# Kernel tuning notes

Measured on AMD Instinct MI355X. Metric: run time of the kernel, lower is better.

Reference implementation:

```python
import itertools
import jax, jax.numpy as jnp
import numpy as np

# static block configuration
B, C, H, W, DIM, HEADS = 2, 4, 60, 120, 512, 8
WS = (2, 6, 12)          # window size (Wc, Wh, Ww)
SS = (1, 3, 6)           # shift size
N = WS[0] * WS[1] * WS[2]            # 144 tokens per window
C1, H1, W1 = C // WS[0], H // WS[1], W // WS[2]
NW = C1 * H1 * W1                    # windows per sample
DH = DIM // HEADS
EPS = 1e-6


def _attn_bias():
    """Static shifted-window attention bias (nW, N, N): 0 within group, -inf across.
    Mirrors compute_3d_shifted_window_mask (warped=True, longitude wrap merge)."""
    img = np.zeros((C, H, W), np.int32)
    c_sl = ((0, C - WS[0]), (C - WS[0], C - SS[0]), (C - SS[0], C))
    h_sl = ((0, H - WS[1]), (H - WS[1], H - SS[1]), (H - SS[1], H))
    w_sl = ((0, W - WS[2]), (W - WS[2], W - SS[2]), (W - SS[2], W))
    cnt = 0
    for (cs, ce), (hs, he), (ws_, we) in itertools.product(c_sl, h_sl, w_sl):
        img[cs:ce, hs:he, ws_:we] = cnt
        cnt += 1
    # warped (periodic longitude) group merges
    for i in range(3):
        for a, b in ((1, 2), (4, 5), (7, 8)):
            img[img == a + 9 * i] = b + 9 * i
    m = img.reshape(C1, WS[0], H1, WS[1], W1, WS[2])
    m = m.transpose(0, 2, 4, 1, 3, 5).reshape(NW, N)
    diff = m[:, None, :] - m[:, :, None]
    return jnp.asarray(np.where(diff != 0, -np.inf, 0.0).astype(np.float32))


_BIAS = _attn_bias()[None, :, None, :, :]  # (1, nW, 1, N, N)


def _ln(x, s, b):
    mu = x.mean(-1, keepdims=True)
    var = x.var(-1, keepdims=True)
    return (x - mu) / jnp.sqrt(var + EPS) * s + b


def setup_inputs() -> dict:
    key = jax.random.key(0)
    ks = jax.random.split(key, 6)
    s = 0.02
    return {
        "x": jax.random.normal(ks[0], (B, C * H * W, DIM), jnp.float32),
        "qkv_w": jax.random.normal(ks[1], (DIM, 3 * DIM), jnp.float32) * s,
        "qkv_b": jnp.zeros((3 * DIM,), jnp.float32),
        "proj_w": jax.random.normal(ks[2], (DIM, DIM), jnp.float32) * s,
        "proj_b": jnp.zeros((DIM,), jnp.float32),
        "norm1_scale": jnp.ones((DIM,), jnp.float32),
        "norm1_bias": jnp.zeros((DIM,), jnp.float32),
        "norm2_scale": jnp.ones((DIM,), jnp.float32),
        "norm2_bias": jnp.zeros((DIM,), jnp.float32),
        "mlp_w1": jax.random.normal(ks[3], (DIM, 4 * DIM), jnp.float32) * s,
        "mlp_b1": jnp.zeros((4 * DIM,), jnp.float32),
        "mlp_w2": jax.random.normal(ks[4], (4 * DIM, DIM), jnp.float32) * s,
        "mlp_b2": jnp.zeros((DIM,), jnp.float32),
    }


def reference(x, qkv_w, qkv_b, proj_w, proj_b, norm1_scale, norm1_bias,
              norm2_scale, norm2_bias, mlp_w1, mlp_b1, mlp_w2, mlp_b2):
    shortcut = x                                   # (B, L, D)
    h = _ln(x, norm1_scale, norm1_bias).reshape(B, C, H, W, DIM)
    # cyclic shift
    h = jnp.roll(h, (-SS[0], -SS[1], -SS[2]), axis=(1, 2, 3))
    # window partition: (B,C,H,W,D) -> (B*nW, N, D)
    h = h.reshape(B, C1, WS[0], H1, WS[1], W1, WS[2], DIM)
    h = h.transpose(0, 1, 3, 5, 2, 4, 6, 7).reshape(B * NW, N, DIM)
    # windowed multi-head self-attention
    qkv = h @ qkv_w + qkv_b                        # (B*nW, N, 3*D)
    qkv = qkv.reshape(B, NW, N, 3, HEADS, DH)
    q = qkv[..., 0, :, :].transpose(0, 1, 3, 2, 4)  # (B, nW, H, N, Dh)
    k = qkv[..., 1, :, :].transpose(0, 1, 3, 2, 4)
    v = qkv[..., 2, :, :].transpose(0, 1, 3, 2, 4)
    scale = 1.0 / float(np.sqrt(DH))
    attn = jnp.einsum("bwhnd,bwhmd->bwhnm", q, k) * scale + _BIAS
    attn = jax.nn.softmax(attn, axis=-1)
    o = jnp.einsum("bwhnm,bwhmd->bwhnd", attn, v)
    o = o.transpose(0, 1, 3, 2, 4).reshape(B * NW, N, DIM)
    o = o @ proj_w + proj_b
    # window reverse: (B*nW, N, D) -> (B,C,H,W,D)
    o = o.reshape(B, C1, H1, W1, WS[0], WS[1], WS[2], DIM)
    o = o.transpose(0, 1, 4, 2, 5, 3, 6, 7).reshape(B, C, H, W, DIM)
    # reverse cyclic shift
    o = jnp.roll(o, SS, axis=(1, 2, 3))
    x = shortcut + o.reshape(B, C * H * W, DIM)    # drop_path is identity
    # MLP block
    h2 = _ln(x, norm2_scale, norm2_bias)
    h2 = jax.nn.gelu(h2 @ mlp_w1 + mlp_b1) @ mlp_w2 + mlp_b2
    return x + h2
```

## Files before the change

### kernel.cpp

```cpp
#include <hip/hip_runtime.h>

typedef __attribute__((ext_vector_type(8))) short bf16x8;
typedef __attribute__((ext_vector_type(4))) float f32x4;
typedef __attribute__((ext_vector_type(8))) unsigned short u16x8;

__device__ inline unsigned short f2bf(float f) {
  unsigned int u = __float_as_uint(f);
  u += 0x7fffu + ((u >> 16) & 1u);
  return (unsigned short)(u >> 16);
}

__device__ inline void gload_lds16(const void* g, void* l) {
  __builtin_amdgcn_global_load_lds(
      (const __attribute__((address_space(1))) void*)g,
      (__attribute__((address_space(3))) void*)l, 16, 0, 0);
}

__global__ void wtrans(const float* __restrict__ W, unsigned short* __restrict__ Wt,
                       int K, int N) {
  int idx = blockIdx.x * 256 + threadIdx.x;
  if (idx >= K * N) return;
  int k = idx / N, n = idx - k * N;
  Wt[(size_t)n * K + k] = f2bf(W[idx]);
}

template <int MODE>
__global__ void ln_k(const float* __restrict__ x, const float* __restrict__ sc,
                     const float* __restrict__ bi, unsigned short* __restrict__ o) {
  int t = blockIdx.x * 4 + (threadIdx.x >> 6);
  int l = threadIdx.x & 63;
  size_t src;
  if (MODE == 0) {
    int b = t / 28800, r = t - b * 28800;
    int win = r / 144, tok = r - win * 144;
    int c1 = win / 100, rem = win - c1 * 100;
    int h1 = rem / 10, w1 = rem - h1 * 10;
    int tc = tok / 72, tr = tok - tc * 72;
    int th = tr / 12, tw = tr - th * 12;
    int cs = c1 * 2 + tc, hs = h1 * 6 + th, wsp = w1 * 12 + tw;
    int co = (cs + 1) & 3;
    int ho = hs + 3; if (ho >= 60) ho -= 60;
    int wo = wsp + 6; if (wo >= 120) wo -= 120;
    src = ((size_t)b * 28800 + (co * 60 + ho) * 120 + wo) * 512;
  } else {
    src = (size_t)t * 512;
  }
  const float4* xr = (const float4*)(x + src);
  float4 v0 = xr[l * 2], v1 = xr[l * 2 + 1];
  float s = v0.x + v0.y + v0.z + v0.w + v1.x + v1.y + v1.z + v1.w;
  float s2 = v0.x * v0.x + v0.y * v0.y + v0.z * v0.z + v0.w * v0.w +
             v1.x * v1.x + v1.y * v1.y + v1.z * v1.z + v1.w * v1.w;
  #pragma unroll
  for (int o2 = 32; o2; o2 >>= 1) {
    s += __shfl_xor(s, o2);
    s2 += __shfl_xor(s2, o2);
  }
  float mean = s * (1.0f / 512.0f);
  float var = s2 * (1.0f / 512.0f) - mean * mean;
  float inv = rsqrtf(var + 1e-6f);
  const float4* scp = (const float4*)sc;
  const float4* bip = (const float4*)bi;
  float4 sa = scp[l * 2], sb = scp[l * 2 + 1];
  float4 ba = bip[l * 2], bb = bip[l * 2 + 1];
  u16x8 ov;
  ov[0] = f2bf((v0.x - mean) * inv * sa.x + ba.x);
  ov[1] = f2bf((v0.y - mean) * inv * sa.y + ba.y);
  ov[2] = f2bf((v0.z - mean) * inv * sa.z + ba.z);
  ov[3] = f2bf((v0.w - mean) * inv * sa.w + ba.w);
  ov[4] = f2bf((v1.x - mean) * inv * sb.x + bb.x);
  ov[5] = f2bf((v1.y - mean) * inv * sb.y + bb.y);
  ov[6] = f2bf((v1.z - mean) * inv * sb.z + bb.z);
  ov[7] = f2bf((v1.w - mean) * inv * sb.w + bb.w);
  *(u16x8*)&o[(size_t)t * 512 + l * 8] = ov;
}

template <int EPI>
__launch_bounds__(256)
__global__ void gemm128(const unsigned short* __restrict__ A,
                        const unsigned short* __restrict__ Bt,
                        const float* __restrict__ bias, void* __restrict__ outp,
                        const float* __restrict__ res, int M, int N, int K) {
  __shared__ __attribute__((aligned(16))) unsigned short As[128 * 32];
  __shared__ __attribute__((aligned(16))) unsigned short Bs[128 * 32];
  int tid = threadIdx.x;
  int w = tid >> 6, l = tid & 63;
  int ntile = N >> 7;
  int bm = blockIdx.x / ntile, bn = blockIdx.x - bm * ntile;
  const unsigned short* Ab = A + (size_t)bm * 128 * K;
  const unsigned short* Bb = Bt + (size_t)bn * 128 * K;
  int lr = l >> 2, lc = (l & 3) << 3;
  int lane15 = l & 15, lk = (l >> 4) << 3;
  int wr = (w >> 1) << 6, wc = (w & 1) << 6;
  f32x4 acc[4][4] = {};
  for (int k0 = 0; k0 < K; k0 += 32) {
    #pragma unroll
    for (int i = 0; i < 2; ++i) {
      int row = i * 64 + w * 16 + lr;
      gload_lds16(Ab + (size_t)row * K + k0 + lc, &As[(i * 64 + w * 16) * 32]);
      gload_lds16(Bb + (size_t)row * K + k0 + lc, &Bs[(i * 64 + w * 16) * 32]);
    }
    __syncthreads();
    bf16x8 af[4], bf[4];
    #pragma unroll
    for (int mt = 0; mt < 4; ++mt)
      af[mt] = *(const bf16x8*)&As[(wr + mt * 16 + lane15) * 32 + lk];
    #pragma unroll
    for (int nt = 0; nt < 4; ++nt)
      bf[nt] = *(const bf16x8*)&Bs[(wc + nt * 16 + lane15) * 32 + lk];
    #pragma unroll
    for (int mt = 0; mt < 4; ++mt)
      #pragma unroll
      for (int nt = 0; nt < 4; ++nt)
        acc[mt][nt] =
            __builtin_amdgcn_mfma_f32_16x16x32_bf16(af[mt], bf[nt], acc[mt][nt], 0, 0, 0);
    __syncthreads();
  }
  float* outf = (float*)outp;
  unsigned short* outh = (unsigned short*)outp;
  #pragma unroll
  for (int mt = 0; mt < 4; ++mt) {
    #pragma unroll
    for (int j = 0; j < 4; ++j) {
      int grow = bm * 128 + wr + mt * 16 + ((l >> 4) << 2) + j;
      int win = 0, tok = 0;
      size_t rowbase = 0;
      if constexpr (EPI == 0) {
        win = grow / 144;
        tok = grow - win * 144;
      } else if constexpr (EPI == 1) {
        win = grow / 144;
        tok = grow - win * 144;
        int b = win / 200, wl = win - b * 200;
        int c1 = wl / 100, rem = wl - c1 * 100;
        int h1 = rem / 10, w1 = rem - h1 * 10;
        int tc = tok / 72, tr = tok - tc * 72;
        int th = tr / 12, tw = tr - th * 12;
        int cs = c1 * 2 + tc, hs = h1 * 6 + th, wsp = w1 * 12 + tw;
        int co = (cs + 1) & 3;
        int ho = hs + 3; if (ho >= 60) ho -= 60;
        int wo = wsp + 6; if (wo >= 120) wo -= 120;
        rowbase = ((size_t)b * 28800 + (co * 60 + ho) * 120 + wo) * 512;
      }
      #pragma unroll
      for (int nt = 0; nt < 4; ++nt) {
        int gcol = bn * 128 + wc + nt * 16 + lane15;
        float val = acc[mt][nt][j] + bias[gcol];
        if constexpr (EPI == 0) {
          int which = gcol >> 9, hd = (gcol >> 6) & 7, dh = gcol & 63;
          outh[(((size_t)(win * 3 + which) * 8 + hd) * 144 + tok) * 64 + dh] = f2bf(val);
        } else if constexpr (EPI == 1) {
          size_t oi = rowbase + gcol;
          outf[oi] = res[oi] + val;
        } else if constexpr (EPI == 2) {
          float u = 0.7978845608f * (val + 0.044715f * val * val * val);
          float g = 0.5f * val * (1.0f + tanhf(u));
          outh[(size_t)grow * N + gcol] = f2bf(g);
        } else {
          size_t oi = (size_t)grow * N + gcol;
          outf[oi] += val;
        }
      }
    }
  }
}

__launch_bounds__(576)
__global__ void attn_k(const unsigned short* __restrict__ qkv,
                       unsigned short* __restrict__ owin) {
  __shared__ __attribute__((aligned(16))) unsigned short Ks[144 * 72];
  __shared__ __attribute__((aligned(16))) unsigned short Vt[64 * 168];
  __shared__ __attribute__((aligned(16))) unsigned short Ps[144 * 168];
  __shared__ unsigned char gid[144];
  int bid = blockIdx.x;
  int win = bid >> 3, head = bid & 7;
  const unsigned short* qb = qkv + ((size_t)(win * 3 + 0) * 8 + head) * (144 * 64);
  const unsigned short* kb = qkv + ((size_t)(win * 3 + 1) * 8 + head) * (144 * 64);
  const unsigned short* vb = qkv + ((size_t)(win * 3 + 2) * 8 + head) * (144 * 64);
  int tid = threadIdx.x;
  {
    int row = tid >> 2, c0 = (tid & 3) << 4;
    u16x8 ka = *(const u16x8*)(kb + row * 64 + c0);
    u16x8 kc = *(const u16x8*)(kb + row * 64 + c0 + 8);
    *(u16x8*)&Ks[row * 72 + c0] = ka;
    *(u16x8*)&Ks[row * 72 + c0 + 8] = kc;
    u16x8 va = *(const u16x8*)(vb + row * 64 + c0);
    u16x8 vc = *(const u16x8*)(vb + row * 64 + c0 + 8);
    #pragma unroll
    for (int j = 0; j < 8; ++j) Vt[(c0 + j) * 168 + row] = va[j];
    #pragma unroll
    for (int j = 0; j < 8; ++j) Vt[(c0 + 8 + j) * 168 + row] = vc[j];
  }
  for (int i = tid; i < 64 * 24; i += 576) {
    int d = i / 24, m = i - d * 24;
    Vt[d * 168 + 144 + m] = 0;
  }
  for (int i = tid; i < 144 * 24; i += 576) {
    int r = i / 24, c = i - r * 24;
    Ps[r * 168 + 144 + c] = 0;
  }
  if (tid < 144) {
    int wl = win % 200;
    int c1 = wl / 100, rem = wl - c1 * 100;
    int h1 = rem / 10, w1 = rem - h1 * 10;
    int tc = tid / 72, tr = tid - tc * 72;
    int th = tr / 12, tw = tr - th * 12;
    int cs = c1 * 2 + tc, hs = h1 * 6 + th, wsp = w1 * 12 + tw;
    int rc = cs < 2 ? 0 : (cs < 3 ? 1 : 2);
    int rh = hs < 54 ? 0 : (hs < 57 ? 1 : 2);
    int rw = wsp < 108 ? 0 : (wsp < 114 ? 1 : 2);
    if (rw == 1) rw = 2;
    gid[tid] = (unsigned char)(rc * 9 + rh * 3 + rw);
  }
  __syncthreads();
  int wv = tid >> 6, l = tid & 63;
  int lane15 = l & 15, lk = (l >> 4) << 3;
  bf16x8 aq0 = *(const bf16x8*)(qb + (wv * 16 + lane15) * 64 + lk);
  bf16x8 aq1 = *(const bf16x8*)(qb + (wv * 16 + lane15) * 64 + 32 + lk);
  f32x4 sf[9];
  #pragma unroll
  for (int ct = 0; ct < 9; ++ct) {
    f32x4 z = {};
    bf16x8 b0 = *(const bf16x8*)&Ks[(ct * 16 + lane15) * 72 + lk];
    bf16x8 b1 = *(const bf16x8*)&Ks[(ct * 16 + lane15) * 72 + 32 + lk];
    z = __builtin_amdgcn_mfma_f32_16x16x32_bf16(aq0, b0, z, 0, 0, 0);
    z = __builtin_amdgcn_mfma_f32_16x16x32_bf16(aq1, b1, z, 0, 0, 0);
    sf[ct] = z;
  }
  int gi[4];
  #pragma unroll
  for (int j = 0; j < 4; ++j) gi[j] = gid[wv * 16 + ((l >> 4) << 2) + j];
  float mx[4] = {-1e30f, -1e30f, -1e30f, -1e30f};
  #pragma unroll
  for (int ct = 0; ct < 9; ++ct) {
    int gj = gid[ct * 16 + lane15];
    #pragma unroll
    for (int j = 0; j < 4; ++j) {
      float s = sf[ct][j] * 0.125f;
      if (gj != gi[j]) s = -1e30f;
      sf[ct][j] = s;
      mx[j] = fmaxf(mx[j], s);
    }
  }
  #pragma unroll
  for (int o2 = 8; o2; o2 >>= 1)
    #pragma unroll
    for (int j = 0; j < 4; ++j) mx[j] = fmaxf(mx[j], __shfl_xor(mx[j], o2));
  float sm[4] = {0.f, 0.f, 0.f, 0.f};
  #pragma unroll
  for (int ct = 0; ct < 9; ++ct)
    #pragma unroll
    for (int j = 0; j < 4; ++j) {
      float e = __expf(sf[ct][j] - mx[j]);
      sf[ct][j] = e;
      sm[j] += e;
    }
  #pragma unroll
  for (int o2 = 8; o2; o2 >>= 1)
    #pragma unroll
    for (int j = 0; j < 4; ++j) sm[j] += __shfl_xor(sm[j], o2);
  float rs[4];
  #pragma unroll
  for (int j = 0; j < 4; ++j) rs[j] = 1.0f / sm[j];
  #pragma unroll
  for (int ct = 0; ct < 9; ++ct)
    #pragma unroll
    for (int j = 0; j < 4; ++j)
      Ps[(wv * 16 + ((l >> 4) << 2) + j) * 168 + ct * 16 + lane15] =
          f2bf(sf[ct][j] * rs[j]);
  __syncthreads();
  f32x4 of[4] = {};
  #pragma unroll
  for (int ks = 0; ks < 5; ++ks) {
    bf16x8 ap = *(const bf16x8*)&Ps[(wv * 16 + lane15) * 168 + ks * 32 + lk];
    #pragma unroll
    for (int nt = 0; nt < 4; ++nt) {
      bf16x8 bv = *(const bf16x8*)&Vt[(nt * 16 + lane15) * 168 + ks * 32 + lk];
      of[nt] = __builtin_amdgcn_mfma_f32_16x16x32_bf16(ap, bv, of[nt], 0, 0, 0);
    }
  }
  unsigned short* ob = owin + (size_t)win * 144 * 512 + head * 64;
  #pragma unroll
  for (int nt = 0; nt < 4; ++nt)
    #pragma unroll
    for (int j = 0; j < 4; ++j) {
      int row = wv * 16 + ((l >> 4) << 2) + j;
      ob[(size_t)row * 512 + nt * 16 + lane15] = f2bf(of[nt][j]);
    }
}

extern "C" void kernel_launch(void* const* d_in, const int* in_sizes, int n_in,
                              void* d_out, int out_size, void* d_ws, size_t ws_size,
                              hipStream_t stream) {
  const float* x = (const float*)d_in[0];
  const float* qkv_w = (const float*)d_in[1];
  const float* qkv_b = (const float*)d_in[2];
  const float* proj_w = (const float*)d_in[3];
  const float* proj_b = (const float*)d_in[4];
  const float* n1s = (const float*)d_in[5];
  const float* n1b = (const float*)d_in[6];
  const float* n2s = (const float*)d_in[7];
  const float* n2b = (const float*)d_in[8];
  const float* w1 = (const float*)d_in[9];
  const float* b1 = (const float*)d_in[10];
  const float* w2 = (const float*)d_in[11];
  const float* b2 = (const float*)d_in[12];
  float* out = (float*)d_out;
  char* ws = (char*)d_ws;

  unsigned short* WqT = (unsigned short*)(ws);
  unsigned short* WpT = (unsigned short*)(ws + 1572864);
  unsigned short* W1T = (unsigned short*)(ws + 2097152);
  unsigned short* W2T = (unsigned short*)(ws + 4194304);
  unsigned short* hwin = (unsigned short*)(ws + 6291456);
  unsigned short* qkvb = (unsigned short*)(ws + 65273856);
  unsigned short* owin = (unsigned short*)(ws + 242221056);
  unsigned short* mid = qkvb;

  wtrans<<<(512 * 1536 + 255) / 256, 256, 0, stream>>>(qkv_w, WqT, 512, 1536);
  wtrans<<<(512 * 512 + 255) / 256, 256, 0, stream>>>(proj_w, WpT, 512, 512);
  wtrans<<<(512 * 2048 + 255) / 256, 256, 0, stream>>>(w1, W1T, 512, 2048);
  wtrans<<<(2048 * 512 + 255) / 256, 256, 0, stream>>>(w2, W2T, 2048, 512);
  ln_k<0><<<14400, 256, 0, stream>>>(x, n1s, n1b, hwin);
  gemm128<0><<<450 * 12, 256, 0, stream>>>(hwin, WqT, qkv_b, qkvb, nullptr, 57600, 1536, 512);
  attn_k<<<3200, 576, 0, stream>>>(qkvb, owin);
  gemm128<1><<<450 * 4, 256, 0, stream>>>(owin, WpT, proj_b, out, x, 57600, 512, 512);
  ln_k<1><<<14400, 256, 0, stream>>>(out, n2s, n2b, hwin);
  gemm128<2><<<450 * 16, 256, 0, stream>>>(hwin, W1T, b1, mid, nullptr, 57600, 2048, 512);
  gemm128<3><<<450 * 4, 256, 0, stream>>>(mid, W2T, b2, out, nullptr, 57600, 512, 2048);
}
```

Measured before the change: 951.1 us.

## Replace 128x128 GEMM with pipelined 256x256 tile GEMM using swizzled LDS

Replaces the simple synchronous 128x128-tile bf16 MFMA GEMM with a 256x256-tile, 512-thread kernel. It uses a 4-deep LDS ring buffer fed by direct global-to-LDS loads, explicit vmcnt waits and barriers, an XOR swizzle on LDS addresses to avoid bank conflicts, and s_setprio around the MFMA bursts. The aim is to overlap global loads with matrix math and raise data reuse per tile, at the cost of more LDS and registers per block and fewer blocks in flight. The GELU tanh is also rewritten in an equivalent exp-based form.

```diff
diff --git a/kernel.cpp b/kernel.cpp
--- a/kernel.cpp
+++ b/kernel.cpp
@@ -3,6 +3,9 @@
 typedef __attribute__((ext_vector_type(8))) short bf16x8;
 typedef __attribute__((ext_vector_type(4))) float f32x4;
 typedef __attribute__((ext_vector_type(8))) unsigned short u16x8;
+
+#define BARX() asm volatile("s_barrier" ::: "memory")
+#define VMC(n) asm volatile("s_waitcnt vmcnt(" #n ")" ::: "memory")
 
 __device__ inline unsigned short f2bf(float f) {
   unsigned int u = __float_as_uint(f);
@@ -75,53 +78,104 @@
 }
 
 template <int EPI>
-__launch_bounds__(256)
-__global__ void gemm128(const unsigned short* __restrict__ A,
+__launch_bounds__(512, 2)
+__global__ void gemm256(const unsigned short* __restrict__ A,
                         const unsigned short* __restrict__ Bt,
                         const float* __restrict__ bias, void* __restrict__ outp,
                         const float* __restrict__ res, int M, int N, int K) {
-  __shared__ __attribute__((aligned(16))) unsigned short As[128 * 32];
-  __shared__ __attribute__((aligned(16))) unsigned short Bs[128 * 32];
-  int tid = threadIdx.x;
-  int w = tid >> 6, l = tid & 63;
-  int ntile = N >> 7;
-  int bm = blockIdx.x / ntile, bn = blockIdx.x - bm * ntile;
-  const unsigned short* Ab = A + (size_t)bm * 128 * K;
-  const unsigned short* Bb = Bt + (size_t)bn * 128 * K;
-  int lr = l >> 2, lc = (l & 3) << 3;
-  int lane15 = l & 15, lk = (l >> 4) << 3;
-  int wr = (w >> 1) << 6, wc = (w & 1) << 6;
-  f32x4 acc[4][4] = {};
-  for (int k0 = 0; k0 < K; k0 += 32) {
+  __shared__ __attribute__((aligned(16))) unsigned short lds[4][2][8192];
+  const int tid = threadIdx.x;
+  const int w = tid >> 6, l = tid & 63;
+  const int wm = w >> 2, wn = w & 3;
+  const int lane15 = l & 15, lk = (l >> 4) << 3;
+  const int ntile = N >> 8;
+  const int bm = blockIdx.x / ntile, bn = blockIdx.x - bm * ntile;
+  const int KT = K >> 6;
+  const unsigned short* Ag = A + (size_t)bm * 256 * K;
+  const unsigned short* Bg = Bt + (size_t)bn * 256 * K;
+  const int lq = l >> 2;
+  const int sc0 = (l & 3) << 3;
+
+  f32x4 acc[8][4] = {};
+
+  auto STAGE = [&](int c, int part) {
+    const unsigned short* gb = part ? Bg : Ag;
+    unsigned short* lb = (unsigned short*)&lds[c & 3][part][0];
+    const int kc = c << 5;
     #pragma unroll
     for (int i = 0; i < 2; ++i) {
-      int row = i * 64 + w * 16 + lr;
-      gload_lds16(Ab + (size_t)row * K + k0 + lc, &As[(i * 64 + w * 16) * 32]);
-      gload_lds16(Bb + (size_t)row * K + k0 + lc, &Bs[(i * 64 + w * 16) * 32]);
-    }
-    __syncthreads();
-    bf16x8 af[4], bf[4];
-    #pragma unroll
-    for (int mt = 0; mt < 4; ++mt)
-      af[mt] = *(const bf16x8*)&As[(wr + mt * 16 + lane15) * 32 + lk];
-    #pragma unroll
-    for (int nt = 0; nt < 4; ++nt)
-      bf[nt] = *(const bf16x8*)&Bs[(wc + nt * 16 + lane15) * 32 + lk];
-    #pragma unroll
-    for (int mt = 0; mt < 4; ++mt)
+      int j = i * 8 + w;
+      int row = j * 16 + lq;
+      int sc = sc0 ^ (((row >> 1) & 3) << 3);
+      gload_lds16(gb + (size_t)row * K + kc + sc, lb + j * 512);
+    }
+  };
+  auto LDA4 = [&](bf16x8* af, int c, int mq) {
+    const unsigned short* p = &lds[c & 3][0][0];
+    #pragma unroll
+    for (int mf = 0; mf < 4; ++mf) {
+      int row = wm * 128 + (mq * 4 + mf) * 16 + lane15;
+      af[mf] = *(const bf16x8*)&p[row * 32 + (lk ^ (((row >> 1) & 3) << 3))];
+    }
+  };
+  auto LDB4 = [&](bf16x8* bfr, int c) {
+    const unsigned short* p = &lds[c & 3][1][0];
+    #pragma unroll
+    for (int nf = 0; nf < 4; ++nf) {
+      int row = wn * 64 + nf * 16 + lane15;
+      bfr[nf] = *(const bf16x8*)&p[row * 32 + (lk ^ (((row >> 1) & 3) << 3))];
+    }
+  };
+  auto MFMA16 = [&](bf16x8* af, bf16x8* bfr, int mq) {
+    __builtin_amdgcn_s_setprio(1);
+    #pragma unroll
+    for (int mf = 0; mf < 4; ++mf)
       #pragma unroll
-      for (int nt = 0; nt < 4; ++nt)
-        acc[mt][nt] =
-            __builtin_amdgcn_mfma_f32_16x16x32_bf16(af[mt], bf[nt], acc[mt][nt], 0, 0, 0);
-    __syncthreads();
-  }
+      for (int nf = 0; nf < 4; ++nf)
+        acc[mq * 4 + mf][nf] = __builtin_amdgcn_mfma_f32_16x16x32_bf16(
+            af[mf], bfr[nf], acc[mq * 4 + mf][nf], 0, 0, 0);
+    __builtin_amdgcn_s_setprio(0);
+  };
+
+  STAGE(0, 0); STAGE(0, 1); STAGE(1, 0); STAGE(1, 1); STAGE(2, 0); STAGE(2, 1);
+  VMC(8);
+  BARX();
+
+  for (int t = 0; t < KT; ++t) {
+    const int c0 = 2 * t, c1 = c0 + 1;
+    const bool s01 = (t <= KT - 2), s23 = (t <= KT - 3);
+    bf16x8 af[4], bfr[4];
+    LDA4(af, c0, 0); LDB4(bfr, c0);
+    if (s01) STAGE(c0 + 3, 0);
+    BARX();
+    MFMA16(af, bfr, 0);
+    BARX();
+    LDA4(af, c0, 1);
+    if (s01) STAGE(c0 + 3, 1);
+    BARX();
+    MFMA16(af, bfr, 1);
+    if (t <= KT - 2) { VMC(8); } else { VMC(0); }
+    BARX();
+    LDA4(af, c1, 0); LDB4(bfr, c1);
+    if (s23) STAGE(c0 + 4, 0);
+    BARX();
+    MFMA16(af, bfr, 0);
+    BARX();
+    LDA4(af, c1, 1);
+    if (s23) STAGE(c0 + 4, 1);
+    BARX();
+    MFMA16(af, bfr, 1);
+    if (s23) { VMC(8); } else if (t == KT - 2) { VMC(4); }
+    BARX();
+  }
+
   float* outf = (float*)outp;
   unsigned short* outh = (unsigned short*)outp;
   #pragma unroll
-  for (int mt = 0; mt < 4; ++mt) {
+  for (int mi = 0; mi < 8; ++mi) {
     #pragma unroll
     for (int j = 0; j < 4; ++j) {
-      int grow = bm * 128 + wr + mt * 16 + ((l >> 4) << 2) + j;
+      int grow = bm * 256 + wm * 128 + mi * 16 + ((l >> 4) << 2) + j;
       int win = 0, tok = 0;
       size_t rowbase = 0;
       if constexpr (EPI == 0) {
@@ -142,9 +196,9 @@
         rowbase = ((size_t)b * 28800 + (co * 60 + ho) * 120 + wo) * 512;
       }
       #pragma unroll
-      for (int nt = 0; nt < 4; ++nt) {
-        int gcol = bn * 128 + wc + nt * 16 + lane15;
-        float val = acc[mt][nt][j] + bias[gcol];
+      for (int nf = 0; nf < 4; ++nf) {
+        int gcol = bn * 256 + wn * 64 + nf * 16 + lane15;
+        float val = acc[mi][nf][j] + bias[gcol];
         if constexpr (EPI == 0) {
           int which = gcol >> 9, hd = (gcol >> 6) & 7, dh = gcol & 63;
           outh[(((size_t)(win * 3 + which) * 8 + hd) * 144 + tok) * 64 + dh] = f2bf(val);
@@ -153,7 +207,7 @@
           outf[oi] = res[oi] + val;
         } else if constexpr (EPI == 2) {
           float u = 0.7978845608f * (val + 0.044715f * val * val * val);
-          float g = 0.5f * val * (1.0f + tanhf(u));
+          float g = val / (1.0f + __expf(-2.0f * u));
           outh[(size_t)grow * N + gcol] = f2bf(g);
         } else {
           size_t oi = (size_t)grow * N + gcol;
@@ -321,10 +375,10 @@
   wtrans<<<(512 * 2048 + 255) / 256, 256, 0, stream>>>(w1, W1T, 512, 2048);
   wtrans<<<(2048 * 512 + 255) / 256, 256, 0, stream>>>(w2, W2T, 2048, 512);
   ln_k<0><<<14400, 256, 0, stream>>>(x, n1s, n1b, hwin);
-  gemm128<0><<<450 * 12, 256, 0, stream>>>(hwin, WqT, qkv_b, qkvb, nullptr, 57600, 1536, 512);
+  gemm256<0><<<225 * 6, 512, 0, stream>>>(hwin, WqT, qkv_b, qkvb, nullptr, 57600, 1536, 512);
   attn_k<<<3200, 576, 0, stream>>>(qkvb, owin);
-  gemm128<1><<<450 * 4, 256, 0, stream>>>(owin, WpT, proj_b, out, x, 57600, 512, 512);
+  gemm256<1><<<225 * 2, 512, 0, stream>>>(owin, WpT, proj_b, out, x, 57600, 512, 512);
   ln_k<1><<<14400, 256, 0, stream>>>(out, n2s, n2b, hwin);
-  gemm128<2><<<450 * 16, 256, 0, stream>>>(hwin, W1T, b1, mid, nullptr, 57600, 2048, 512);
-  gemm128<3><<<450 * 4, 256, 0, stream>>>(mid, W2T, b2, out, nullptr, 57600, 512, 2048);
-}
+  gemm256<2><<<225 * 8, 512, 0, stream>>>(hwin, W1T, b1, mid, nullptr, 57600, 2048, 512);
+  gemm256<3><<<225 * 2, 512, 0, stream>>>(mid, W2T, b2, out, nullptr, 57600, 512, 2048);
+}
```

Result: no change. 933.3 us (-1.9%).

## Rewrite GEMM as 128x256 tile with triple-buffered LDS pipeline and XCD remap

Applied to the files above, without the earlier changes.

Replaces the 128x128 single-buffered GEMM with a 128x256 tile kernel. It triple-buffers LDS via async global-to-LDS loads with explicit vmcnt waits, uses swizzled LDS addressing with inline ds_read_b128, and interleaves MFMA with s_setprio. Blocks are remapped across the 8 XCDs for L2 locality, and the GELU tanh is replaced by an equivalent sigmoid form using __expf. The aim is to hide global load latency, cut barrier overhead and raise MFMA utilisation, at the cost of more registers and LDS (72KB per block) and fragile hand-written waitcnt logic.

```diff
diff --git a/kernel.cpp b/kernel.cpp
--- a/kernel.cpp
+++ b/kernel.cpp
@@ -3,6 +3,13 @@
 typedef __attribute__((ext_vector_type(8))) short bf16x8;
 typedef __attribute__((ext_vector_type(4))) float f32x4;
 typedef __attribute__((ext_vector_type(8))) unsigned short u16x8;
+
+#define BAR() __builtin_amdgcn_s_barrier()
+#define VMC(n) asm volatile("s_waitcnt vmcnt(" #n ")" ::: "memory")
+#define SB0() __builtin_amdgcn_sched_barrier(0)
+#define WAITL() do { asm volatile("s_waitcnt lgkmcnt(0)"); SB0(); } while (0)
+#define DSRI(dst, base, imm) \
+  asm volatile("ds_read_b128 %0, %1 offset:%2" : "=&v"(dst) : "v"(base), "i"(imm))
 
 __device__ inline unsigned short f2bf(float f) {
   unsigned int u = __float_as_uint(f);
@@ -75,53 +82,109 @@
 }
 
 template <int EPI>
-__launch_bounds__(256)
-__global__ void gemm128(const unsigned short* __restrict__ A,
-                        const unsigned short* __restrict__ Bt,
-                        const float* __restrict__ bias, void* __restrict__ outp,
-                        const float* __restrict__ res, int M, int N, int K) {
-  __shared__ __attribute__((aligned(16))) unsigned short As[128 * 32];
-  __shared__ __attribute__((aligned(16))) unsigned short Bs[128 * 32];
-  int tid = threadIdx.x;
-  int w = tid >> 6, l = tid & 63;
-  int ntile = N >> 7;
-  int bm = blockIdx.x / ntile, bn = blockIdx.x - bm * ntile;
-  const unsigned short* Ab = A + (size_t)bm * 128 * K;
-  const unsigned short* Bb = Bt + (size_t)bn * 128 * K;
-  int lr = l >> 2, lc = (l & 3) << 3;
-  int lane15 = l & 15, lk = (l >> 4) << 3;
-  int wr = (w >> 1) << 6, wc = (w & 1) << 6;
-  f32x4 acc[4][4] = {};
-  for (int k0 = 0; k0 < K; k0 += 32) {
-    #pragma unroll
-    for (int i = 0; i < 2; ++i) {
-      int row = i * 64 + w * 16 + lr;
-      gload_lds16(Ab + (size_t)row * K + k0 + lc, &As[(i * 64 + w * 16) * 32]);
-      gload_lds16(Bb + (size_t)row * K + k0 + lc, &Bs[(i * 64 + w * 16) * 32]);
-    }
-    __syncthreads();
-    bf16x8 af[4], bf[4];
-    #pragma unroll
-    for (int mt = 0; mt < 4; ++mt)
-      af[mt] = *(const bf16x8*)&As[(wr + mt * 16 + lane15) * 32 + lk];
-    #pragma unroll
-    for (int nt = 0; nt < 4; ++nt)
-      bf[nt] = *(const bf16x8*)&Bs[(wc + nt * 16 + lane15) * 32 + lk];
-    #pragma unroll
-    for (int mt = 0; mt < 4; ++mt)
+__launch_bounds__(256, 2)
+__global__ void gemmT(const unsigned short* __restrict__ A,
+                      const unsigned short* __restrict__ Bt,
+                      const float* __restrict__ bias, void* __restrict__ outp,
+                      const float* __restrict__ res, int M, int N, int K) {
+  __shared__ __attribute__((aligned(16))) unsigned short lds3[3][12288];
+  const int tid = threadIdx.x;
+  const int w = tid >> 6, l = tid & 63;
+  const int lane15 = l & 15, lk = (l >> 4) << 3;
+  const int ntile = N >> 8;
+  const int nwg = gridDim.x;
+  const int q = nwg >> 3, r = nwg & 7;
+  const int xcd = blockIdx.x & 7, idx8 = blockIdx.x >> 3;
+  const int wgid = (xcd < r ? xcd * (q + 1) : r * (q + 1) + (xcd - r) * q) + idx8;
+  const int bm = wgid / ntile, bn = wgid - bm * ntile;
+  const int KT = K >> 5;
+
+  const int swzb = ((l >> 3) & 3) << 3;
+  const int colx = (((l & 3) << 3) ^ swzb);
+  const int rA0 = (0 * 4 + w) * 16 + (l >> 2);
+  const int rA1 = (1 * 4 + w) * 16 + (l >> 2);
+  const int offA0 = (rA0 * K + colx) * 2, offA1 = (rA1 * K + colx) * 2;
+  int offB[4];
+  #pragma unroll
+  for (int j = 0; j < 4; ++j)
+    offB[j] = (((j * 4 + w) * 16 + (l >> 2)) * K + colx) * 2;
+
+  const int sw = ((lane15 >> 1) & 3) << 3;
+  unsigned lds0 = (unsigned)(unsigned long long)
+      (__attribute__((address_space(3))) void*)(void*)&lds3[0][0];
+  const unsigned comA = (unsigned)(lane15 * 64 + ((lk ^ sw) << 1));
+  unsigned bA0 = lds0 + comA;
+  unsigned bA1 = bA0 + 24576u, bA2 = bA0 + 49152u;
+  const unsigned bOffB = 8192u + ((unsigned)w << 12);
+  unsigned bB0 = bA0 + bOffB, bB1 = bA1 + bOffB, bB2 = bA2 + bOffB;
+
+  unsigned short* p0 = &lds3[0][0];
+  unsigned short* p1 = &lds3[1][0];
+  unsigned short* p2 = &lds3[2][0];
+
+  const char* gA = (const char*)(A + (size_t)bm * 128 * K);
+  const char* gB = (const char*)(Bt + (size_t)bn * 256 * K);
+
+  f32x4 acc[8][4] = {};
+  bf16x8 afL[4], afH[4], bfr[4];
+
+  auto STAGE = [&](unsigned short* pS, const char* ga, const char* gb) {
+    gload_lds16(ga + offA0, pS + w * 512);
+    gload_lds16(ga + offA1, pS + 2048 + w * 512);
+    #pragma unroll
+    for (int j = 0; j < 4; ++j)
+      gload_lds16(gb + offB[j], pS + 4096 + (j * 4 + w) * 512);
+  };
+
+  STAGE(p0, gA, gB); gA += 64; gB += 64;
+  STAGE(p1, gA, gB); gA += 64; gB += 64;
+  VMC(6);
+  BAR();
+
+  for (int t = 0; t < KT; ++t) {
+    DSRI(afL[0], bA0, 0);    DSRI(afL[1], bA0, 1024);
+    DSRI(afL[2], bA0, 2048); DSRI(afL[3], bA0, 3072);
+    DSRI(bfr[0], bB0, 0);    DSRI(bfr[1], bB0, 1024);
+    DSRI(bfr[2], bB0, 2048); DSRI(bfr[3], bB0, 3072);
+    if (t < KT - 2) {
+      STAGE(p2, gA, gB);
+      gA += 64; gB += 64;
+    }
+    WAITL();
+    DSRI(afH[0], bA0, 4096); DSRI(afH[1], bA0, 5120);
+    DSRI(afH[2], bA0, 6144); DSRI(afH[3], bA0, 7168);
+    SB0();
+    __builtin_amdgcn_s_setprio(1);
+    #pragma unroll
+    for (int mf = 0; mf < 4; ++mf)
       #pragma unroll
-      for (int nt = 0; nt < 4; ++nt)
-        acc[mt][nt] =
-            __builtin_amdgcn_mfma_f32_16x16x32_bf16(af[mt], bf[nt], acc[mt][nt], 0, 0, 0);
-    __syncthreads();
-  }
+      for (int nf = 0; nf < 4; ++nf)
+        acc[mf][nf] = __builtin_amdgcn_mfma_f32_16x16x32_bf16(
+            afL[mf], bfr[nf], acc[mf][nf], 0, 0, 0);
+    __builtin_amdgcn_s_setprio(0);
+    WAITL();
+    __builtin_amdgcn_s_setprio(1);
+    #pragma unroll
+    for (int mf = 0; mf < 4; ++mf)
+      #pragma unroll
+      for (int nf = 0; nf < 4; ++nf)
+        acc[4 + mf][nf] = __builtin_amdgcn_mfma_f32_16x16x32_bf16(
+            afH[mf], bfr[nf], acc[4 + mf][nf], 0, 0, 0);
+    __builtin_amdgcn_s_setprio(0);
+    if (t < KT - 2) { VMC(6); } else if (t == KT - 2) { VMC(0); }
+    if (t < KT - 1) BAR();
+    unsigned ta = bA0; bA0 = bA1; bA1 = bA2; bA2 = ta;
+    unsigned tb = bB0; bB0 = bB1; bB1 = bB2; bB2 = tb;
+    unsigned short* tp = p0; p0 = p1; p1 = p2; p2 = tp;
+  }
+
   float* outf = (float*)outp;
   unsigned short* outh = (unsigned short*)outp;
   #pragma unroll
-  for (int mt = 0; mt < 4; ++mt) {
+  for (int mi = 0; mi < 8; ++mi) {
     #pragma unroll
     for (int j = 0; j < 4; ++j) {
-      int grow = bm * 128 + wr + mt * 16 + ((l >> 4) << 2) + j;
+      int grow = bm * 128 + mi * 16 + ((l >> 4) << 2) + j;
       int win = 0, tok = 0;
       size_t rowbase = 0;
       if constexpr (EPI == 0) {
@@ -142,9 +205,9 @@
         rowbase = ((size_t)b * 28800 + (co * 60 + ho) * 120 + wo) * 512;
       }
       #pragma unroll
-      for (int nt = 0; nt < 4; ++nt) {
-        int gcol = bn * 128 + wc + nt * 16 + lane15;
-        float val = acc[mt][nt][j] + bias[gcol];
+      for (int nf = 0; nf < 4; ++nf) {
+        int gcol = bn * 256 + w * 64 + nf * 16 + lane15;
+        float val = acc[mi][nf][j] + bias[gcol];
         if constexpr (EPI == 0) {
           int which = gcol >> 9, hd = (gcol >> 6) & 7, dh = gcol & 63;
           outh[(((size_t)(win * 3 + which) * 8 + hd) * 144 + tok) * 64 + dh] = f2bf(val);
@@ -153,7 +216,7 @@
           outf[oi] = res[oi] + val;
         } else if constexpr (EPI == 2) {
           float u = 0.7978845608f * (val + 0.044715f * val * val * val);
-          float g = 0.5f * val * (1.0f + tanhf(u));
+          float g = val / (1.0f + __expf(-2.0f * u));
           outh[(size_t)grow * N + gcol] = f2bf(g);
         } else {
           size_t oi = (size_t)grow * N + gcol;
@@ -321,10 +384,10 @@
   wtrans<<<(512 * 2048 + 255) / 256, 256, 0, stream>>>(w1, W1T, 512, 2048);
   wtrans<<<(2048 * 512 + 255) / 256, 256, 0, stream>>>(w2, W2T, 2048, 512);
   ln_k<0><<<14400, 256, 0, stream>>>(x, n1s, n1b, hwin);
-  gemm128<0><<<450 * 12, 256, 0, stream>>>(hwin, WqT, qkv_b, qkvb, nullptr, 57600, 1536, 512);
+  gemmT<0><<<450 * 6, 256, 0, stream>>>(hwin, WqT, qkv_b, qkvb, nullptr, 57600, 1536, 512);
   attn_k<<<3200, 576, 0, stream>>>(qkvb, owin);
-  gemm128<1><<<450 * 4, 256, 0, stream>>>(owin, WpT, proj_b, out, x, 57600, 512, 512);
+  gemmT<1><<<450 * 2, 256, 0, stream>>>(owin, WpT, proj_b, out, x, 57600, 512, 512);
   ln_k<1><<<14400, 256, 0, stream>>>(out, n2s, n2b, hwin);
-  gemm128<2><<<450 * 16, 256, 0, stream>>>(hwin, W1T, b1, mid, nullptr, 57600, 2048, 512);
-  gemm128<3><<<450 * 4, 256, 0, stream>>>(mid, W2T, b2, out, nullptr, 57600, 512, 2048);
-}
+  gemmT<2><<<450 * 8, 256, 0, stream>>>(hwin, W1T, b1, mid, nullptr, 57600, 2048, 512);
+  gemmT<3><<<450 * 2, 256, 0, stream>>>(mid, W2T, b2, out, nullptr, 57600, 512, 2048);
+}
```

Result: faster. 793.1 us (-16.6%).

## Switch GEMMs to fragment-tiled operand layout with register-resident A and XCD remap

Applied to the files above, without the earlier changes.

Producers (LayerNorm, attention output, GELU epilogue) and the weight transpose now write operands directly in an MFMA fragment-tiled layout. A new GEMM keeps A fragments in registers, loaded straight from global memory with double buffering, and stages only B segments in LDS. Each workgroup covers 512 rows by 64 columns, and workgroup IDs are remapped across XCDs for locality. GELU uses an exp-based sigmoid form instead of tanhf. The cost is higher register pressure, a larger LDS footprint, and clamped redundant work for tail waves.

```diff
diff --git a/kernel.cpp b/kernel.cpp
--- a/kernel.cpp
+++ b/kernel.cpp
@@ -3,6 +3,9 @@
 typedef __attribute__((ext_vector_type(8))) short bf16x8;
 typedef __attribute__((ext_vector_type(4))) float f32x4;
 typedef __attribute__((ext_vector_type(8))) unsigned short u16x8;
+
+#define BAR() __builtin_amdgcn_s_barrier()
+#define VMC(n) asm volatile("s_waitcnt vmcnt(" #n ")" ::: "memory")
 
 __device__ inline unsigned short f2bf(float f) {
   unsigned int u = __float_as_uint(f);
@@ -16,12 +19,18 @@
       (__attribute__((address_space(3))) void*)l, 16, 0, 0);
 }
 
-__global__ void wtrans(const float* __restrict__ W, unsigned short* __restrict__ Wt,
-                       int K, int N) {
+__global__ void wtrans_ft(const float* __restrict__ W, unsigned short* __restrict__ Bft,
+                          int K, int N) {
   int idx = blockIdx.x * 256 + threadIdx.x;
-  if (idx >= K * N) return;
-  int k = idx / N, n = idx - k * N;
-  Wt[(size_t)n * K + k] = f2bf(W[idx]);
+  if (idx >= N * (K >> 3)) return;
+  int n = idx % N, k8 = idx / N;
+  int k0 = k8 << 3;
+  u16x8 ov;
+  #pragma unroll
+  for (int i = 0; i < 8; ++i) ov[i] = f2bf(W[(size_t)(k0 + i) * N + n]);
+  size_t dst = ((size_t)(k0 >> 5) * (N >> 4) + (n >> 4)) * 512 +
+               (((n & 15) | (((k0 >> 3) & 3) << 4)) << 3);
+  *(u16x8*)&Bft[dst] = ov;
 }
 
 template <int MODE>
@@ -71,57 +80,116 @@
   ov[5] = f2bf((v1.y - mean) * inv * sb.y + bb.y);
   ov[6] = f2bf((v1.z - mean) * inv * sb.z + bb.z);
   ov[7] = f2bf((v1.w - mean) * inv * sb.w + bb.w);
-  *(u16x8*)&o[(size_t)t * 512 + l * 8] = ov;
+  size_t dst = ((size_t)(l >> 2) * 3600 + (t >> 4)) * 512 +
+               (((t & 15) | ((l & 3) << 4)) << 3);
+  *(u16x8*)&o[dst] = ov;
 }
 
 template <int EPI>
-__launch_bounds__(256)
-__global__ void gemm128(const unsigned short* __restrict__ A,
-                        const unsigned short* __restrict__ Bt,
-                        const float* __restrict__ bias, void* __restrict__ outp,
-                        const float* __restrict__ res, int M, int N, int K) {
-  __shared__ __attribute__((aligned(16))) unsigned short As[128 * 32];
-  __shared__ __attribute__((aligned(16))) unsigned short Bs[128 * 32];
-  int tid = threadIdx.x;
-  int w = tid >> 6, l = tid & 63;
-  int ntile = N >> 7;
-  int bm = blockIdx.x / ntile, bn = blockIdx.x - bm * ntile;
-  const unsigned short* Ab = A + (size_t)bm * 128 * K;
-  const unsigned short* Bb = Bt + (size_t)bn * 128 * K;
-  int lr = l >> 2, lc = (l & 3) << 3;
-  int lane15 = l & 15, lk = (l >> 4) << 3;
-  int wr = (w >> 1) << 6, wc = (w & 1) << 6;
-  f32x4 acc[4][4] = {};
-  for (int k0 = 0; k0 < K; k0 += 32) {
-    #pragma unroll
-    for (int i = 0; i < 2; ++i) {
-      int row = i * 64 + w * 16 + lr;
-      gload_lds16(Ab + (size_t)row * K + k0 + lc, &As[(i * 64 + w * 16) * 32]);
-      gload_lds16(Bb + (size_t)row * K + k0 + lc, &Bs[(i * 64 + w * 16) * 32]);
-    }
-    __syncthreads();
-    bf16x8 af[4], bf[4];
-    #pragma unroll
-    for (int mt = 0; mt < 4; ++mt)
-      af[mt] = *(const bf16x8*)&As[(wr + mt * 16 + lane15) * 32 + lk];
-    #pragma unroll
-    for (int nt = 0; nt < 4; ++nt)
-      bf[nt] = *(const bf16x8*)&Bs[(wc + nt * 16 + lane15) * 32 + lk];
-    #pragma unroll
-    for (int mt = 0; mt < 4; ++mt)
-      #pragma unroll
-      for (int nt = 0; nt < 4; ++nt)
-        acc[mt][nt] =
-            __builtin_amdgcn_mfma_f32_16x16x32_bf16(af[mt], bf[nt], acc[mt][nt], 0, 0, 0);
-    __syncthreads();
-  }
+__launch_bounds__(256, 2)
+__global__ void gemmF(const unsigned short* __restrict__ Aft,
+                      const unsigned short* __restrict__ Bft,
+                      const float* __restrict__ bias, void* __restrict__ outp,
+                      const float* __restrict__ res, int Mreal, int N, int K) {
+  __shared__ __attribute__((aligned(16))) unsigned short ldsB[32768];
+  const int tid = threadIdx.x;
+  const int w = tid >> 6, l = tid & 63;
+  const int lane15 = l & 15;
+  const int nt = N >> 6;
+  const int nwg = gridDim.x;
+  const int q = nwg >> 3, r = nwg & 7;
+  const int xcd = blockIdx.x & 7, idx8 = blockIdx.x >> 3;
+  const int wgid = (xcd < r ? xcd * (q + 1) : r * (q + 1) + (xcd - r) * q) + idx8;
+  const int bm = wgid / nt, bn = wgid - bm * nt;
+  const int KC = K >> 5;
+  const int NSEG = K >> 9;
+  const size_t aStep = (size_t)(Mreal >> 4) * 512;
+
+  int rb = bm * 512 + w * 128;
+  const bool wactive = rb < Mreal;
+  if (!wactive) rb = Mreal - 128;
+
+  const unsigned short* pW = Aft + (size_t)(rb >> 4) * 512 + (size_t)l * 8;
+
+  auto STAGE_SEG = [&](int s) {
+    #pragma unroll
+    for (int rr = 0; rr < 16; ++rr) {
+      size_t srcb = ((size_t)(s * 16 + rr) * (N >> 4) + bn * 4) * 512 + tid * 8;
+      gload_lds16(Bft + srcb, &ldsB[rr * 2048 + w * 512]);
+    }
+  };
+
+  f32x4 acc[8][4] = {};
+  bf16x8 a0[8], a1[8];
+
+  STAGE_SEG(0);
+  #pragma unroll
+  for (int mi = 0; mi < 8; ++mi) a0[mi] = *(const bf16x8*)(pW + mi * 512);
+  #pragma unroll
+  for (int mi = 0; mi < 8; ++mi) a1[mi] = *(const bf16x8*)(pW + aStep + mi * 512);
+  const unsigned short* pPre = pW + 2 * aStep;
+  VMC(0);
+  BAR();
+
+  for (int s = 0; s < NSEG; ++s) {
+    if (s) {
+      BAR();
+      STAGE_SEG(s);
+      VMC(0);
+      BAR();
+    }
+    const int cbase = s * 16;
+    #pragma unroll
+    for (int k2 = 0; k2 < 8; ++k2) {
+      {
+        const int kl = 2 * k2;
+        bf16x8 b0 = *(const bf16x8*)&ldsB[kl * 2048 + 0 * 512 + l * 8];
+        bf16x8 b1 = *(const bf16x8*)&ldsB[kl * 2048 + 1 * 512 + l * 8];
+        bf16x8 b2 = *(const bf16x8*)&ldsB[kl * 2048 + 2 * 512 + l * 8];
+        bf16x8 b3 = *(const bf16x8*)&ldsB[kl * 2048 + 3 * 512 + l * 8];
+        #pragma unroll
+        for (int mi = 0; mi < 8; ++mi) {
+          acc[mi][0] = __builtin_amdgcn_mfma_f32_16x16x32_bf16(a0[mi], b0, acc[mi][0], 0, 0, 0);
+          acc[mi][1] = __builtin_amdgcn_mfma_f32_16x16x32_bf16(a0[mi], b1, acc[mi][1], 0, 0, 0);
+          acc[mi][2] = __builtin_amdgcn_mfma_f32_16x16x32_bf16(a0[mi], b2, acc[mi][2], 0, 0, 0);
+          acc[mi][3] = __builtin_amdgcn_mfma_f32_16x16x32_bf16(a0[mi], b3, acc[mi][3], 0, 0, 0);
+        }
+        if (cbase + kl + 2 < KC) {
+          #pragma unroll
+          for (int mi = 0; mi < 8; ++mi) a0[mi] = *(const bf16x8*)(pPre + mi * 512);
+          pPre += aStep;
+        }
+      }
+      {
+        const int kl = 2 * k2 + 1;
+        bf16x8 b0 = *(const bf16x8*)&ldsB[kl * 2048 + 0 * 512 + l * 8];
+        bf16x8 b1 = *(const bf16x8*)&ldsB[kl * 2048 + 1 * 512 + l * 8];
+        bf16x8 b2 = *(const bf16x8*)&ldsB[kl * 2048 + 2 * 512 + l * 8];
+        bf16x8 b3 = *(const bf16x8*)&ldsB[kl * 2048 + 3 * 512 + l * 8];
+        #pragma unroll
+        for (int mi = 0; mi < 8; ++mi) {
+          acc[mi][0] = __builtin_amdgcn_mfma_f32_16x16x32_bf16(a1[mi], b0, acc[mi][0], 0, 0, 0);
+          acc[mi][1] = __builtin_amdgcn_mfma_f32_16x16x32_bf16(a1[mi], b1, acc[mi][1], 0, 0, 0);
+          acc[mi][2] = __builtin_amdgcn_mfma_f32_16x16x32_bf16(a1[mi], b2, acc[mi][2], 0, 0, 0);
+          acc[mi][3] = __builtin_amdgcn_mfma_f32_16x16x32_bf16(a1[mi], b3, acc[mi][3], 0, 0, 0);
+        }
+        if (cbase + kl + 2 < KC) {
+          #pragma unroll
+          for (int mi = 0; mi < 8; ++mi) a1[mi] = *(const bf16x8*)(pPre + mi * 512);
+          pPre += aStep;
+        }
+      }
+    }
+  }
+
+  if (!wactive) return;
   float* outf = (float*)outp;
   unsigned short* outh = (unsigned short*)outp;
   #pragma unroll
-  for (int mt = 0; mt < 4; ++mt) {
+  for (int mi = 0; mi < 8; ++mi) {
     #pragma unroll
     for (int j = 0; j < 4; ++j) {
-      int grow = bm * 128 + wr + mt * 16 + ((l >> 4) << 2) + j;
+      int grow = rb + mi * 16 + ((l >> 4) << 2) + j;
       int win = 0, tok = 0;
       size_t rowbase = 0;
       if constexpr (EPI == 0) {
@@ -142,9 +210,9 @@
         rowbase = ((size_t)b * 28800 + (co * 60 + ho) * 120 + wo) * 512;
       }
       #pragma unroll
-      for (int nt = 0; nt < 4; ++nt) {
-        int gcol = bn * 128 + wc + nt * 16 + lane15;
-        float val = acc[mt][nt][j] + bias[gcol];
+      for (int nf = 0; nf < 4; ++nf) {
+        int gcol = bn * 64 + nf * 16 + lane15;
+        float val = acc[mi][nf][j] + bias[gcol];
         if constexpr (EPI == 0) {
           int which = gcol >> 9, hd = (gcol >> 6) & 7, dh = gcol & 63;
           outh[(((size_t)(win * 3 + which) * 8 + hd) * 144 + tok) * 64 + dh] = f2bf(val);
@@ -153,8 +221,10 @@
           outf[oi] = res[oi] + val;
         } else if constexpr (EPI == 2) {
           float u = 0.7978845608f * (val + 0.044715f * val * val * val);
-          float g = 0.5f * val * (1.0f + tanhf(u));
-          outh[(size_t)grow * N + gcol] = f2bf(g);
+          float g = val / (1.0f + __expf(-2.0f * u));
+          size_t dst = ((size_t)(gcol >> 5) * 3600 + (grow >> 4)) * 512 +
+                       (((grow & 15) | (((gcol >> 3) & 3) << 4)) << 3) + (gcol & 7);
+          outh[dst] = f2bf(g);
         } else {
           size_t oi = (size_t)grow * N + gcol;
           outf[oi] += val;
@@ -278,13 +348,15 @@
       of[nt] = __builtin_amdgcn_mfma_f32_16x16x32_bf16(ap, bv, of[nt], 0, 0, 0);
     }
   }
-  unsigned short* ob = owin + (size_t)win * 144 * 512 + head * 64;
   #pragma unroll
   for (int nt = 0; nt < 4; ++nt)
     #pragma unroll
     for (int j = 0; j < 4; ++j) {
-      int row = wv * 16 + ((l >> 4) << 2) + j;
-      ob[(size_t)row * 512 + nt * 16 + lane15] = f2bf(of[nt][j]);
+      int row = win * 144 + wv * 16 + ((l >> 4) << 2) + j;
+      int col = head * 64 + nt * 16 + lane15;
+      size_t dst = ((size_t)(col >> 5) * 3600 + (row >> 4)) * 512 +
+                   (((row & 15) | (((col >> 3) & 3) << 4)) << 3) + (col & 7);
+      owin[dst] = f2bf(of[nt][j]);
     }
 }
 
@@ -316,15 +388,15 @@
   unsigned short* owin = (unsigned short*)(ws + 242221056);
   unsigned short* mid = qkvb;
 
-  wtrans<<<(512 * 1536 + 255) / 256, 256, 0, stream>>>(qkv_w, WqT, 512, 1536);
-  wtrans<<<(512 * 512 + 255) / 256, 256, 0, stream>>>(proj_w, WpT, 512, 512);
-  wtrans<<<(512 * 2048 + 255) / 256, 256, 0, stream>>>(w1, W1T, 512, 2048);
-  wtrans<<<(2048 * 512 + 255) / 256, 256, 0, stream>>>(w2, W2T, 2048, 512);
+  wtrans_ft<<<(1536 * 64 + 255) / 256, 256, 0, stream>>>(qkv_w, WqT, 512, 1536);
+  wtrans_ft<<<(512 * 64 + 255) / 256, 256, 0, stream>>>(proj_w, WpT, 512, 512);
+  wtrans_ft<<<(2048 * 64 + 255) / 256, 256, 0, stream>>>(w1, W1T, 512, 2048);
+  wtrans_ft<<<(512 * 256 + 255) / 256, 256, 0, stream>>>(w2, W2T, 2048, 512);
   ln_k<0><<<14400, 256, 0, stream>>>(x, n1s, n1b, hwin);
-  gemm128<0><<<450 * 12, 256, 0, stream>>>(hwin, WqT, qkv_b, qkvb, nullptr, 57600, 1536, 512);
+  gemmF<0><<<113 * 24, 256, 0, stream>>>(hwin, WqT, qkv_b, qkvb, nullptr, 57600, 1536, 512);
   attn_k<<<3200, 576, 0, stream>>>(qkvb, owin);
-  gemm128<1><<<450 * 4, 256, 0, stream>>>(owin, WpT, proj_b, out, x, 57600, 512, 512);
+  gemmF<1><<<113 * 8, 256, 0, stream>>>(owin, WpT, proj_b, out, x, 57600, 512, 512);
   ln_k<1><<<14400, 256, 0, stream>>>(out, n2s, n2b, hwin);
-  gemm128<2><<<450 * 16, 256, 0, stream>>>(hwin, W1T, b1, mid, nullptr, 57600, 2048, 512);
-  gemm128<3><<<450 * 4, 256, 0, stream>>>(mid, W2T, b2, out, nullptr, 57600, 512, 2048);
-}
+  gemmF<2><<<113 * 32, 256, 0, stream>>>(hwin, W1T, b1, mid, nullptr, 57600, 2048, 512);
+  gemmF<3><<<113 * 8, 256, 0, stream>>>(mid, W2T, b2, out, nullptr, 57600, 512, 2048);
+}
```

After: 997.8 us. 1.05x slower.
